# Kernel optimization log

Measured on AMD Instinct MI355X. Metric: run time of the kernel, lower is better.

## Reference

```python
import jax, jax.numpy as jnp
import numpy as np

NUM_HEADS = 4
WORD_DIM = 100
LEAKY_ALPHA = 0.3  # keras LeakyReLU default negative_slope


def setup_inputs() -> dict:
    key = jax.random.key(0)
    k1, k2, k3 = jax.random.split(key, 3)
    x = jax.random.normal(k1, (8, 30, 20, 40, WORD_DIM), dtype=jnp.float32)
    # keras 'random_normal' initializer: stddev 0.05
    w_att = jax.random.normal(k2, (NUM_HEADS, WORD_DIM), dtype=jnp.float32) * 0.05
    b_att = jax.random.normal(k3, (NUM_HEADS, WORD_DIM), dtype=jnp.float32) * 0.05
    return {"x": x, "w_att": w_att, "b_att": b_att}


def reference(x, w_att, b_att):
    # x: [B, T, E, W, D]; w_att, b_att: [H, D]
    B, T, E, W, D = x.shape
    H = w_att.shape[0]
    type_emb = x[..., 0, :]        # [B,T,E,D]
    words = x[..., 1:, :]          # [B,T,E,N,D], N = W-1
    # per-head hidden representation: leaky_relu(w*words + b)
    pre = words[..., None, :, :] * w_att[:, None, :] + b_att[:, None, :]  # [B,T,E,H,N,D]
    hidden = jnp.where(pre >= 0, pre, LEAKY_ALPHA * pre)
    # attention scores: dot(type_emb, hidden) over D
    scores = jnp.einsum('bted,btehnd->btehn', type_emb, hidden)  # [B,T,E,H,N]
    # original uses raw exp / sum (no max-subtraction) -- keep faithful
    att = jnp.exp(scores)
    att = att / jnp.sum(att, axis=-1, keepdims=True)
    out = jnp.einsum('btehn,btend->bthed'.replace('bthed', 'btehd'), att, words)  # [B,T,E,H,D]
    out = out.reshape(B, T, E, H * D)
    # all-zero events map to zero embeddings
    nonzero = jnp.any(x != 0, axis=(-1, -2), keepdims=False)  # [B,T,E]
    out = jnp.where(nonzero[..., None], out, 0.0)
    return out
```

## Files before the change

### kernel.cpp

```cpp
#include <hip/hip_runtime.h>
#include <math.h>
#include <stdint.h>

#define NHEAD 4
#define DD 100
#define NW 39
#define BLOCK 128

typedef float v2f __attribute__((ext_vector_type(2)));
typedef __attribute__((address_space(3))) uint32_t lds_t;
typedef const __attribute__((address_space(1))) uint32_t glb_t;

__global__ __launch_bounds__(BLOCK) void ts_enc(
    const float* __restrict__ x,
    const float* __restrict__ w_att,
    const float* __restrict__ b_att,
    float* __restrict__ out)
{
    __shared__ float tile[40 * DD];

    const int tid  = threadIdx.x;
    const int wv   = __builtin_amdgcn_readfirstlane(tid >> 6);
    const int lane = tid & 63;
    const float* xsite = x + (size_t)blockIdx.x * (40 * DD);

    #pragma unroll
    for (int i = 0; i < 8; ++i) {
        const int cf = i * BLOCK + tid;
        if (cf < 1000) {
            glb_t* g = (glb_t*)(xsite + cf * 4);
            lds_t* l = (lds_t*)(tile + (i * BLOCK + wv * 64) * 4);
            __builtin_amdgcn_global_load_lds(g, l, 16, 0, 0);
        }
    }
    __syncthreads();

    const bool act  = lane < NW;
    const int  nrow = act ? lane : NW - 1;
    const float* wrow = tile + (1 + nrow) * DD;
    const int h0 = wv * 2;

    v2f acA0 = {0,0}, acB0 = {0,0};
    v2f acA1 = {0,0}, acB1 = {0,0};

    #pragma unroll
    for (int c = 0; c < 25; ++c) {
        const v2f x01 = *(const v2f*)(wrow + c * 4);
        const v2f x23 = *(const v2f*)(wrow + c * 4 + 2);
        const v2f t01 = *(const v2f*)(xsite + c * 4);
        const v2f t23 = *(const v2f*)(xsite + c * 4 + 2);
        #pragma unroll
        for (int hh = 0; hh < 2; ++hh) {
            const int h = h0 + hh;
            const v2f w01 = *(const v2f*)(w_att + h * DD + c * 4);
            const v2f w23 = *(const v2f*)(w_att + h * DD + c * 4 + 2);
            const v2f b01 = *(const v2f*)(b_att + h * DD + c * 4);
            const v2f b23 = *(const v2f*)(b_att + h * DD + c * 4 + 2);
            const v2f p01 = x01 * w01 + b01;
            const v2f p23 = x23 * w23 + b23;
            const v2f l01 = __builtin_elementwise_max(p01, 0.3f * p01);
            const v2f l23 = __builtin_elementwise_max(p23, 0.3f * p23);
            if (hh == 0) { acA0 = t01 * l01 + acA0; acB0 = t23 * l23 + acB0; }
            else         { acA1 = t01 * l01 + acA1; acB1 = t23 * l23 + acB1; }
        }
    }
    const float sc0 = (acA0.x + acA0.y) + (acB0.x + acB0.y);
    const float sc1 = (acA1.x + acA1.y) + (acB1.x + acB1.y);

    const float e0 = act ? __expf(sc0) : 0.f;
    const float e1 = act ? __expf(sc1) : 0.f;

    const int l2 = lane < 50 ? lane : 49;
    const float* wb = tile + DD + l2 * 2;
    v2f o0 = {0,0}, o1 = {0,0};
    float s0 = 0.f, s1 = 0.f;
    #pragma unroll
    for (int n = 0; n < NW; ++n) {
        const float a0 = __builtin_bit_cast(float,
            __builtin_amdgcn_readlane(__builtin_bit_cast(int, e0), n));
        const float a1 = __builtin_bit_cast(float,
            __builtin_amdgcn_readlane(__builtin_bit_cast(int, e1), n));
        const v2f wd = *(const v2f*)(wb + n * DD);
        o0 = a0 * wd + o0;
        o1 = a1 * wd + o1;
        s0 += a0;
        s1 += a1;
    }
    const float r0 = 1.f / s0;
    const float r1 = 1.f / s1;
    if (lane < 50) {
        float* ob = out + (size_t)blockIdx.x * (NHEAD * DD) + h0 * DD + lane * 2;
        const v2f q0 = o0 * r0;
        const v2f q1 = o1 * r1;
        *(v2f*)(ob)      = q0;
        *(v2f*)(ob + DD) = q1;
    }
}

extern "C" void kernel_launch(void* const* d_in, const int* in_sizes, int n_in,
                              void* d_out, int out_size, void* d_ws, size_t ws_size,
                              hipStream_t stream) {
    const float* x     = (const float*)d_in[0];
    const float* w_att = (const float*)d_in[1];
    const float* b_att = (const float*)d_in[2];
    float* out = (float*)d_out;

    const int sites = 8 * 30 * 20;
    ts_enc<<<sites, BLOCK, 0, stream>>>(x, w_att, b_att, out);
}
```

Baseline: 32.52 us.

## Stage word rows in LDS as packed bf16 and normalize softmax via wave reduction

Words are now loaded through registers, converted to packed bf16, and stored in a padded LDS layout with a 54-word row stride. This replaces the direct global-to-LDS fp32 copy and halves the LDS footprint, which together with the launch-bounds hint of 8 blocks allows more blocks per CU. The softmax denominator is now computed with a wave shuffle reduction before the weighted sum, removing the per-iteration sum and the final divide. Rounding the words to bf16 loses precision in both the scores and the output, which may exceed tolerance.

```diff
diff --git a/kernel.cpp b/kernel.cpp
--- a/kernel.cpp
+++ b/kernel.cpp
@@ -6,18 +6,17 @@
 #define DD 100
 #define NW 39
 #define BLOCK 128
+#define RW 54
 
 typedef float v2f __attribute__((ext_vector_type(2)));
-typedef __attribute__((address_space(3))) uint32_t lds_t;
-typedef const __attribute__((address_space(1))) uint32_t glb_t;
 
-__global__ __launch_bounds__(BLOCK) void ts_enc(
+__global__ __launch_bounds__(BLOCK, 8) void ts_enc(
     const float* __restrict__ x,
     const float* __restrict__ w_att,
     const float* __restrict__ b_att,
     float* __restrict__ out)
 {
-    __shared__ float tile[40 * DD];
+    __shared__ uint32_t wl[NW * RW];
 
     const int tid  = threadIdx.x;
     const int wv   = __builtin_amdgcn_readfirstlane(tid >> 6);
@@ -26,27 +25,33 @@
 
     #pragma unroll
     for (int i = 0; i < 8; ++i) {
-        const int cf = i * BLOCK + tid;
-        if (cf < 1000) {
-            glb_t* g = (glb_t*)(xsite + cf * 4);
-            lds_t* l = (lds_t*)(tile + (i * BLOCK + wv * 64) * 4);
-            __builtin_amdgcn_global_load_lds(g, l, 16, 0, 0);
+        const int f = i * BLOCK + tid;
+        if (f < 975) {
+            const float4 q = *(const float4*)(xsite + DD + f * 4);
+            const int r = f / 25;
+            const int m = f - r * 25;
+            uint32_t p0, p1;
+            asm("v_cvt_pk_bf16_f32 %0, %1, %2" : "=v"(p0) : "v"(q.x), "v"(q.y));
+            asm("v_cvt_pk_bf16_f32 %0, %1, %2" : "=v"(p1) : "v"(q.z), "v"(q.w));
+            *(uint2*)&wl[r * RW + m * 2] = make_uint2(p0, p1);
         }
     }
     __syncthreads();
 
     const bool act  = lane < NW;
     const int  nrow = act ? lane : NW - 1;
-    const float* wrow = tile + (1 + nrow) * DD;
-    const int h0 = wv * 2;
+    const uint32_t* wr = wl + nrow * RW;
+    const int h0 = 2 * wv;
 
-    v2f acA0 = {0,0}, acB0 = {0,0};
-    v2f acA1 = {0,0}, acB1 = {0,0};
+    v2f ac0A = {0,0}, ac0B = {0,0}, ac1A = {0,0}, ac1B = {0,0};
 
     #pragma unroll
     for (int c = 0; c < 25; ++c) {
-        const v2f x01 = *(const v2f*)(wrow + c * 4);
-        const v2f x23 = *(const v2f*)(wrow + c * 4 + 2);
+        const uint2 v = *(const uint2*)(wr + c * 2);
+        const v2f x01 = { __builtin_bit_cast(float, v.x << 16),
+                          __builtin_bit_cast(float, v.x & 0xFFFF0000u) };
+        const v2f x23 = { __builtin_bit_cast(float, v.y << 16),
+                          __builtin_bit_cast(float, v.y & 0xFFFF0000u) };
         const v2f t01 = *(const v2f*)(xsite + c * 4);
         const v2f t23 = *(const v2f*)(xsite + c * 4 + 2);
         #pragma unroll
@@ -60,40 +65,43 @@
             const v2f p23 = x23 * w23 + b23;
             const v2f l01 = __builtin_elementwise_max(p01, 0.3f * p01);
             const v2f l23 = __builtin_elementwise_max(p23, 0.3f * p23);
-            if (hh == 0) { acA0 = t01 * l01 + acA0; acB0 = t23 * l23 + acB0; }
-            else         { acA1 = t01 * l01 + acA1; acB1 = t23 * l23 + acB1; }
+            if (hh == 0) { ac0A = t01 * l01 + ac0A; ac0B = t23 * l23 + ac0B; }
+            else         { ac1A = t01 * l01 + ac1A; ac1B = t23 * l23 + ac1B; }
         }
     }
-    const float sc0 = (acA0.x + acA0.y) + (acB0.x + acB0.y);
-    const float sc1 = (acA1.x + acA1.y) + (acB1.x + acB1.y);
+    const float sc0 = (ac0A.x + ac0A.y) + (ac0B.x + ac0B.y);
+    const float sc1 = (ac1A.x + ac1A.y) + (ac1B.x + ac1B.y);
 
     const float e0 = act ? __expf(sc0) : 0.f;
     const float e1 = act ? __expf(sc1) : 0.f;
+    float sm0 = e0, sm1 = e1;
+    #pragma unroll
+    for (int off = 32; off; off >>= 1) {
+        sm0 += __shfl_xor(sm0, off);
+        sm1 += __shfl_xor(sm1, off);
+    }
+    const float att0 = e0 * __builtin_amdgcn_rcpf(sm0);
+    const float att1 = e1 * __builtin_amdgcn_rcpf(sm1);
 
     const int l2 = lane < 50 ? lane : 49;
-    const float* wb = tile + DD + l2 * 2;
+    const uint32_t* cb = wl + l2;
     v2f o0 = {0,0}, o1 = {0,0};
-    float s0 = 0.f, s1 = 0.f;
     #pragma unroll
     for (int n = 0; n < NW; ++n) {
+        const uint32_t u = cb[n * RW];
+        const v2f wd = { __builtin_bit_cast(float, u << 16),
+                         __builtin_bit_cast(float, u & 0xFFFF0000u) };
         const float a0 = __builtin_bit_cast(float,
-            __builtin_amdgcn_readlane(__builtin_bit_cast(int, e0), n));
+            __builtin_amdgcn_readlane(__builtin_bit_cast(int, att0), n));
         const float a1 = __builtin_bit_cast(float,
-            __builtin_amdgcn_readlane(__builtin_bit_cast(int, e1), n));
-        const v2f wd = *(const v2f*)(wb + n * DD);
+            __builtin_amdgcn_readlane(__builtin_bit_cast(int, att1), n));
         o0 = a0 * wd + o0;
         o1 = a1 * wd + o1;
-        s0 += a0;
-        s1 += a1;
     }
-    const float r0 = 1.f / s0;
-    const float r1 = 1.f / s1;
     if (lane < 50) {
         float* ob = out + (size_t)blockIdx.x * (NHEAD * DD) + h0 * DD + lane * 2;
-        const v2f q0 = o0 * r0;
-        const v2f q1 = o1 * r1;
-        *(v2f*)(ob)      = q0;
-        *(v2f*)(ob + DD) = q1;
+        *(v2f*)(ob)      = o0;
+        *(v2f*)(ob + DD) = o1;
     }
 }
 
```

New measurement: 38.29 us. +17.8%, slower.

## Split fused attention kernel into score kernel and weighted-sum kernel via workspace

Applied to the files above, without the earlier changes.

Splits the single fused kernel into two launches. The first computes normalized attention weights with one wave per head (256 threads, softmax sum by shuffle) and writes them to workspace. The second has each wave handle one site and all four heads, re-reading x from global memory. This spreads the score work over more waves, at the cost of a second launch, reading x twice, and a workspace round trip.

```diff
diff --git a/kernel.cpp b/kernel.cpp
--- a/kernel.cpp
+++ b/kernel.cpp
@@ -5,17 +5,17 @@
 #define NHEAD 4
 #define DD 100
 #define NW 39
-#define BLOCK 128
+#define SITES 4800
 
 typedef float v2f __attribute__((ext_vector_type(2)));
 typedef __attribute__((address_space(3))) uint32_t lds_t;
 typedef const __attribute__((address_space(1))) uint32_t glb_t;
 
-__global__ __launch_bounds__(BLOCK) void ts_enc(
+__global__ __launch_bounds__(256, 6) void k_att(
     const float* __restrict__ x,
     const float* __restrict__ w_att,
     const float* __restrict__ b_att,
-    float* __restrict__ out)
+    float* __restrict__ att)
 {
     __shared__ float tile[40 * DD];
 
@@ -25,11 +25,11 @@
     const float* xsite = x + (size_t)blockIdx.x * (40 * DD);
 
     #pragma unroll
-    for (int i = 0; i < 8; ++i) {
-        const int cf = i * BLOCK + tid;
+    for (int i = 0; i < 4; ++i) {
+        const int cf = i * 256 + tid;
         if (cf < 1000) {
             glb_t* g = (glb_t*)(xsite + cf * 4);
-            lds_t* l = (lds_t*)(tile + (i * BLOCK + wv * 64) * 4);
+            lds_t* l = (lds_t*)(tile + (i * 256 + wv * 64) * 4);
             __builtin_amdgcn_global_load_lds(g, l, 16, 0, 0);
         }
     }
@@ -38,62 +38,74 @@
     const bool act  = lane < NW;
     const int  nrow = act ? lane : NW - 1;
     const float* wrow = tile + (1 + nrow) * DD;
-    const int h0 = wv * 2;
 
-    v2f acA0 = {0,0}, acB0 = {0,0};
-    v2f acA1 = {0,0}, acB1 = {0,0};
-
+    v2f accA = {0.f, 0.f}, accB = {0.f, 0.f};
     #pragma unroll
     for (int c = 0; c < 25; ++c) {
         const v2f x01 = *(const v2f*)(wrow + c * 4);
         const v2f x23 = *(const v2f*)(wrow + c * 4 + 2);
         const v2f t01 = *(const v2f*)(xsite + c * 4);
         const v2f t23 = *(const v2f*)(xsite + c * 4 + 2);
-        #pragma unroll
-        for (int hh = 0; hh < 2; ++hh) {
-            const int h = h0 + hh;
-            const v2f w01 = *(const v2f*)(w_att + h * DD + c * 4);
-            const v2f w23 = *(const v2f*)(w_att + h * DD + c * 4 + 2);
-            const v2f b01 = *(const v2f*)(b_att + h * DD + c * 4);
-            const v2f b23 = *(const v2f*)(b_att + h * DD + c * 4 + 2);
-            const v2f p01 = x01 * w01 + b01;
-            const v2f p23 = x23 * w23 + b23;
-            const v2f l01 = __builtin_elementwise_max(p01, 0.3f * p01);
-            const v2f l23 = __builtin_elementwise_max(p23, 0.3f * p23);
-            if (hh == 0) { acA0 = t01 * l01 + acA0; acB0 = t23 * l23 + acB0; }
-            else         { acA1 = t01 * l01 + acA1; acB1 = t23 * l23 + acB1; }
-        }
+        const v2f w01 = *(const v2f*)(w_att + wv * DD + c * 4);
+        const v2f w23 = *(const v2f*)(w_att + wv * DD + c * 4 + 2);
+        const v2f b01 = *(const v2f*)(b_att + wv * DD + c * 4);
+        const v2f b23 = *(const v2f*)(b_att + wv * DD + c * 4 + 2);
+        const v2f p01 = x01 * w01 + b01;
+        const v2f p23 = x23 * w23 + b23;
+        const v2f l01 = __builtin_elementwise_max(p01, 0.3f * p01);
+        const v2f l23 = __builtin_elementwise_max(p23, 0.3f * p23);
+        accA = t01 * l01 + accA;
+        accB = t23 * l23 + accB;
     }
-    const float sc0 = (acA0.x + acA0.y) + (acB0.x + acB0.y);
-    const float sc1 = (acA1.x + acA1.y) + (acB1.x + acB1.y);
+    const float sc = (accA.x + accA.y) + (accB.x + accB.y);
 
-    const float e0 = act ? __expf(sc0) : 0.f;
-    const float e1 = act ? __expf(sc1) : 0.f;
+    const float e = act ? __expf(sc) : 0.f;
+    float sm = e;
+    #pragma unroll
+    for (int off = 32; off; off >>= 1) sm += __shfl_xor(sm, off);
+    const float a = e / sm;
+    if (act) att[(size_t)blockIdx.x * 160 + lane * 4 + wv] = a;
+}
+
+__global__ __launch_bounds__(256, 4) void k_out(
+    const float* __restrict__ x,
+    const float* __restrict__ att,
+    float* __restrict__ out)
+{
+    const int tid  = threadIdx.x;
+    const int wv   = __builtin_amdgcn_readfirstlane(tid >> 6);
+    const int lane = tid & 63;
+    const int site = blockIdx.x * 4 + wv;
+
+    const int nl = lane < NW ? lane : NW - 1;
+    const float4 at4 = *(const float4*)(att + (size_t)site * 160 + nl * 4);
 
     const int l2 = lane < 50 ? lane : 49;
-    const float* wb = tile + DD + l2 * 2;
-    v2f o0 = {0,0}, o1 = {0,0};
-    float s0 = 0.f, s1 = 0.f;
+    const float* wb = x + (size_t)site * (40 * DD) + DD + l2 * 2;
+
+    v2f o0 = {0,0}, o1 = {0,0}, o2 = {0,0}, o3 = {0,0};
     #pragma unroll
     for (int n = 0; n < NW; ++n) {
+        const v2f wd = *(const v2f*)(wb + n * DD);
         const float a0 = __builtin_bit_cast(float,
-            __builtin_amdgcn_readlane(__builtin_bit_cast(int, e0), n));
+            __builtin_amdgcn_readlane(__builtin_bit_cast(int, at4.x), n));
         const float a1 = __builtin_bit_cast(float,
-            __builtin_amdgcn_readlane(__builtin_bit_cast(int, e1), n));
-        const v2f wd = *(const v2f*)(wb + n * DD);
+            __builtin_amdgcn_readlane(__builtin_bit_cast(int, at4.y), n));
+        const float a2 = __builtin_bit_cast(float,
+            __builtin_amdgcn_readlane(__builtin_bit_cast(int, at4.z), n));
+        const float a3 = __builtin_bit_cast(float,
+            __builtin_amdgcn_readlane(__builtin_bit_cast(int, at4.w), n));
         o0 = a0 * wd + o0;
         o1 = a1 * wd + o1;
-        s0 += a0;
-        s1 += a1;
+        o2 = a2 * wd + o2;
+        o3 = a3 * wd + o3;
     }
-    const float r0 = 1.f / s0;
-    const float r1 = 1.f / s1;
     if (lane < 50) {
-        float* ob = out + (size_t)blockIdx.x * (NHEAD * DD) + h0 * DD + lane * 2;
-        const v2f q0 = o0 * r0;
-        const v2f q1 = o1 * r1;
-        *(v2f*)(ob)      = q0;
-        *(v2f*)(ob + DD) = q1;
+        float* ob = out + (size_t)site * (NHEAD * DD) + lane * 2;
+        *(v2f*)(ob)          = o0;
+        *(v2f*)(ob + DD)     = o1;
+        *(v2f*)(ob + 2 * DD) = o2;
+        *(v2f*)(ob + 3 * DD) = o3;
     }
 }
 
@@ -104,7 +116,8 @@
     const float* w_att = (const float*)d_in[1];
     const float* b_att = (const float*)d_in[2];
     float* out = (float*)d_out;
+    float* att = (float*)d_ws;
 
-    const int sites = 8 * 30 * 20;
-    ts_enc<<<sites, BLOCK, 0, stream>>>(x, w_att, b_att, out);
+    k_att<<<SITES, 256, 0, stream>>>(x, w_att, b_att, att);
+    k_out<<<SITES / 4, 256, 0, stream>>>(x, att, out);
 }
```

After: 41.03 us. 26.2% more time.
